# Optimization experiments

Measured on AMD Instinct MI355X. Metric: run time of the kernel, lower is better.

The kernel has to match this reference:

```python
import jax, jax.numpy as jnp
import numpy as np
from jax import lax

N_SAMPLES = 2 ** 15      # 32768
D_SIZE = 256             # number of dictionary atoms
KERNEL = 256             # atom length
N_STEPS = 16             # sparse_coding_iterations
CHANNELS = 128


def setup_inputs() -> dict:
    key = jax.random.key(0)
    ks = jax.random.split(key, 9)
    B = 8
    x = jax.random.normal(ks[0], (B, N_SAMPLES), dtype=jnp.float32)
    # dictionary, initialized uniform(-1, 1) as in nn.Parameter(...).uniform_(-1, 1)
    d = jax.random.uniform(ks[1], (D_SIZE, KERNEL), dtype=jnp.float32, minval=-1.0, maxval=1.0)
    # 1x1 Conv1d weights stored as (out, in); biases (out,)
    w_pos_amp = jax.random.normal(ks[2], (CHANNELS, 2), dtype=jnp.float32) * 0.1
    b_pos_amp = jnp.zeros((CHANNELS,), dtype=jnp.float32)
    w_atoms = jax.random.normal(ks[3], (CHANNELS, D_SIZE), dtype=jnp.float32) * 0.05
    b_atoms = jnp.zeros((CHANNELS,), dtype=jnp.float32)
    w_reduce = jax.random.normal(ks[4], (CHANNELS, 2 * CHANNELS), dtype=jnp.float32) * 0.05
    b_reduce = jnp.zeros((CHANNELS,), dtype=jnp.float32)
    return {
        'x': x, 'd': d,
        'w_pos_amp': w_pos_amp, 'b_pos_amp': b_pos_amp,
        'w_atoms': w_atoms, 'b_atoms': b_atoms,
        'w_reduce': w_reduce, 'b_reduce': b_reduce,
    }


def _correlate(residual, d):
    # residual: (B, 1, N), d: (D, K) -> feature map (B, D, N-K+1) (valid cross-correlation,
    # identical to torch F.conv1d with no padding)
    return lax.conv_general_dilated(
        residual, d[:, None, :], window_strides=(1,), padding='VALID',
        dimension_numbers=('NCH', 'OIH', 'NCH'))


def _matching_pursuit(x3, d):
    """16-step greedy matching pursuit. Returns key points (B, 2+D, N_STEPS) and residual."""
    B = x3.shape[0]
    T = N_SAMPLES - KERNEL + 1  # valid correlation length

    def step(residual, _):
        fm = _correlate(residual, d)                       # (B, D, T)
        flat = fm.reshape(B, -1)
        idx = jnp.argmax(jnp.abs(flat), axis=1)            # best (atom, pos) per example
        amp = jnp.take_along_axis(flat, idx[:, None], axis=1)[:, 0]
        atom_idx = idx // T
        pos = idx % T

        def subtract(r, p, ai, a):
            seg = lax.dynamic_slice(r, (p,), (KERNEL,))
            return lax.dynamic_update_slice(r, seg - a * d[ai], (p,))

        new_res = jax.vmap(subtract)(residual[:, 0, :], pos, atom_idx, amp)[:, None, :]
        enc = jnp.concatenate([
            (pos.astype(jnp.float32) / T)[:, None],        # normalized position
            amp[:, None],                                  # amplitude
            jax.nn.one_hot(atom_idx, D_SIZE, dtype=jnp.float32),  # atom one-hot
        ], axis=1)                                         # (B, 2+D)
        return new_res, enc

    residual, encs = lax.scan(step, x3, None, length=N_STEPS)  # encs: (S, B, 2+D)
    kp = jnp.transpose(encs, (1, 2, 0))                        # (B, 2+D, S)
    return kp, residual


def _conv1x1(w, b, x):
    # w: (O, C), x: (B, C, T) -> (B, O, T)
    return jnp.einsum('oc,bct->bot', w, x) + b[None, :, None]


def reference(x, d, w_pos_amp, b_pos_amp, w_atoms, b_atoms, w_reduce, b_reduce):
    B = x.shape[0]
    x3 = x.reshape(B, 1, N_SAMPLES)
    kp, _ = _matching_pursuit(x3, d)          # (B, 258, 16)
    pos_amp = kp[:, :2, :]
    atoms = kp[:, 2:, :]
    pa = _conv1x1(w_pos_amp, b_pos_amp, pos_amp)
    at = _conv1x1(w_atoms, b_atoms, atoms)
    h = jnp.concatenate([pa, at], axis=1)     # (B, 2*channels, 16)
    return _conv1x1(w_reduce, b_reduce, h)    # (B, channels, 16)
```

## Files before the change

kernel.cpp:

```cpp
#include <hip/hip_runtime.h>
#include <hip/hip_bf16.h>
#include <float.h>

#define NS 32768
#define KER 256
#define TOUT 32513
#define NATOM 256
#define NSTEP 16
#define BATCH 8
#define NBLK 255
#define XSTR 33024
#define SW4(i) ((i) + (((i) >> 5) << 2))

typedef __attribute__((ext_vector_type(8))) _Float16 half8;
typedef __attribute__((ext_vector_type(16))) float f32x16;
typedef __attribute__((ext_vector_type(4))) unsigned int uint4v;
typedef unsigned long long u64;

__device__ __forceinline__ void cmax(float& ba, float& bs, float& bi,
                                     float oa, float os, float oi) {
    if (oa > ba || (oa == ba && oi < bi)) { ba = oa; bs = os; bi = oi; }
}

__device__ __forceinline__ u64 packkey(float sig, int idx) {
    return ((u64)__float_as_uint(fabsf(sig)) << 32)
         | ((u64)((0x7FFFFFu - (unsigned int)idx) << 1))
         | (u64)(__float_as_uint(sig) >> 31);
}
__device__ __forceinline__ void unpackkey(u64 k, float& sig, int& idx) {
    const float av = __uint_as_float((unsigned int)(k >> 32));
    const unsigned int lo = (unsigned int)k;
    idx = 0x7FFFFF - (int)((lo >> 1) & 0x7FFFFFu);
    sig = (lo & 1u) ? -av : av;
}

__device__ __forceinline__ void fma8(float acc[8], float4 dA, float4 dB,
                                     float4 w0, float4 w1, float4 w2, float4 w3) {
    float w[16] = {w0.x,w0.y,w0.z,w0.w, w1.x,w1.y,w1.z,w1.w,
                   w2.x,w2.y,w2.z,w2.w, w3.x,w3.y,w3.z,w3.w};
    float dv[8] = {dA.x,dA.y,dA.z,dA.w, dB.x,dB.y,dB.z,dB.w};
#pragma unroll
    for (int i = 0; i < 8; ++i)
#pragma unroll
        for (int j = 0; j < 8; ++j)
            acc[j] = fmaf(dv[i], w[i + j], acc[j]);
}

__device__ __forceinline__ unsigned short f16hi(float v) {
    return __builtin_bit_cast(unsigned short, (_Float16)v);
}
__device__ __forceinline__ unsigned short f16lo(float v) {
    const _Float16 h = (_Float16)v;
    return __builtin_bit_cast(unsigned short, (_Float16)(v - (float)h));
}

__global__ __launch_bounds__(256) void k_prep(const float* __restrict__ x,
                                              const float* __restrict__ d,
                                              uint4* __restrict__ xhl4,
                                              uint4* __restrict__ dhF,
                                              uint4* __restrict__ dlF) {
    const int gid = blockIdx.x * 256 + threadIdx.x;
    const int NXE = BATCH * XSTR;
    if (gid < NXE) {
        const int b = gid / XSTR, i = gid - b * XSTR;
        float v[4];
#pragma unroll
        for (int u = 0; u < 4; ++u)
            v[u] = (i + u < NS) ? x[b * NS + i + u] : 0.f;
        uint4 q;
        q.x = (unsigned int)f16hi(v[0]) | ((unsigned int)f16hi(v[1]) << 16);
        q.y = (unsigned int)f16hi(v[2]) | ((unsigned int)f16hi(v[3]) << 16);
        q.z = (unsigned int)f16lo(v[0]) | ((unsigned int)f16lo(v[1]) << 16);
        q.w = (unsigned int)f16lo(v[2]) | ((unsigned int)f16lo(v[3]) << 16);
        xhl4[gid] = q;
    } else {
        const int j = gid - NXE;
        if (j < NATOM * 32) {
            const int kg = j >> 8, atom = j & 255;
            const float* dp = d + atom * 256 + (kg << 3);
            uint4 hw, lw;
            hw.x = (unsigned int)f16hi(dp[0]) | ((unsigned int)f16hi(dp[1]) << 16);
            hw.y = (unsigned int)f16hi(dp[2]) | ((unsigned int)f16hi(dp[3]) << 16);
            hw.z = (unsigned int)f16hi(dp[4]) | ((unsigned int)f16hi(dp[5]) << 16);
            hw.w = (unsigned int)f16hi(dp[6]) | ((unsigned int)f16hi(dp[7]) << 16);
            lw.x = (unsigned int)f16lo(dp[0]) | ((unsigned int)f16lo(dp[1]) << 16);
            lw.y = (unsigned int)f16lo(dp[2]) | ((unsigned int)f16lo(dp[3]) << 16);
            lw.z = (unsigned int)f16lo(dp[4]) | ((unsigned int)f16lo(dp[5]) << 16);
            lw.w = (unsigned int)f16lo(dp[6]) | ((unsigned int)f16lo(dp[7]) << 16);
            dhF[(kg << 8) + atom] = hw;
            dlF[(kg << 8) + atom] = lw;
        }
    }
}

__global__ __launch_bounds__(256) void k_init(const uint4* __restrict__ xhl4,
                                              const uint4* __restrict__ dhF,
                                              const uint4* __restrict__ dlF,
                                              float2* __restrict__ bm,
                                              u64* __restrict__ l2k) {
    const int c = blockIdx.x, mg = blockIdx.y, b = blockIdx.z;
    const int tid = threadIdx.x;
    const int w = tid >> 6, l = tid & 63;
    const int n = l & 31, h = l >> 5;
    __shared__ uint4 xw[512];
    __shared__ u64 wmax[4][32];
    const int t0 = c << 8;
    xw[tid] = xhl4[b * XSTR + t0 + tid];
    xw[tid + 256] = xhl4[b * XSTR + t0 + 256 + tid];
    __syncthreads();

    f32x16 acc00, acc01;
#pragma unroll
    for (int j = 0; j < 16; ++j) { acc00[j] = 0.f; acc01[j] = 0.f; }

    const int abase = (mg << 5) + n;
    const int sbb = (w << 6) + n + (h << 3);

    half8 fbh[4], fbl[4];
    {
        const uint4 q0 = xw[sbb], q1 = xw[sbb + 4];
        const uint4v hv = {q0.x, q0.y, q1.x, q1.y};
        const uint4v lv = {q0.z, q0.w, q1.z, q1.w};
        fbh[0] = __builtin_bit_cast(half8, hv);
        fbl[0] = __builtin_bit_cast(half8, lv);
    }
    {
        const uint4 q0 = xw[sbb + 16], q1 = xw[sbb + 20];
        const uint4v hv = {q0.x, q0.y, q1.x, q1.y};
        const uint4v lv = {q0.z, q0.w, q1.z, q1.w};
        fbh[1] = __builtin_bit_cast(half8, hv);
        fbl[1] = __builtin_bit_cast(half8, lv);
    }

#pragma unroll 4
    for (int kk = 0; kk < 16; ++kk) {
        const int kg = (kk << 1) + h;
        const half8 ah0 = __builtin_bit_cast(half8, dhF[(kg << 8) + abase]);
        const half8 al0 = __builtin_bit_cast(half8, dlF[(kg << 8) + abase]);
        {
            const int sN = sbb + ((kk + 2) << 4);
            const uint4 q0 = xw[sN], q1 = xw[sN + 4];
            const uint4v hv = {q0.x, q0.y, q1.x, q1.y};
            const uint4v lv = {q0.z, q0.w, q1.z, q1.w};
            fbh[(kk + 2) & 3] = __builtin_bit_cast(half8, hv);
            fbl[(kk + 2) & 3] = __builtin_bit_cast(half8, lv);
        }
        const half8 b0h = fbh[kk & 3],       b0l = fbl[kk & 3];
        const half8 b1h = fbh[(kk + 2) & 3], b1l = fbl[(kk + 2) & 3];
        acc00 = __builtin_amdgcn_mfma_f32_32x32x16_f16(ah0, b0l, acc00, 0, 0, 0);
        acc00 = __builtin_amdgcn_mfma_f32_32x32x16_f16(al0, b0h, acc00, 0, 0, 0);
        acc00 = __builtin_amdgcn_mfma_f32_32x32x16_f16(ah0, b0h, acc00, 0, 0, 0);
        acc01 = __builtin_amdgcn_mfma_f32_32x32x16_f16(ah0, b1l, acc01, 0, 0, 0);
        acc01 = __builtin_amdgcn_mfma_f32_32x32x16_f16(al0, b1h, acc01, 0, 0, 0);
        acc01 = __builtin_amdgcn_mfma_f32_32x32x16_f16(ah0, b1h, acc01, 0, 0, 0);
    }

    const int tb = t0 + (w << 6) + n;
#pragma unroll
    for (int r = 0; r < 16; ++r) {
        const int amt = (r & 3) + ((r >> 2) << 3) + (h << 2);
        const int idx0 = ((mg << 5) + amt) * TOUT + tb;
        const float v0 = acc00[r], v1 = acc01[r];
        const unsigned int c0 = (0x7FFFFFu - (unsigned int)idx0);
        u64 k0 = 0ull, k1 = 0ull;
        if (tb < TOUT)
            k0 = ((u64)__float_as_uint(fabsf(v0)) << 32)
               | ((u64)(c0 << 1))
               | (u64)(__float_as_uint(v0) >> 31);
        if (tb + 32 < TOUT)
            k1 = ((u64)__float_as_uint(fabsf(v1)) << 32)
               | ((u64)((c0 - 32u) << 1))
               | (u64)(__float_as_uint(v1) >> 31);
        u64 k = (k1 > k0) ? k1 : k0;
#pragma unroll
        for (int m = 1; m <= 16; m <<= 1) {
            const u64 ok = __shfl_xor(k, m, 32);
            if (ok > k) k = ok;
        }
        if (n == 0) wmax[w][amt] = k;
    }
    __syncthreads();
    if (tid < 64) {
        const int a = tid & 31, p = tid >> 5;
        u64 k = wmax[(p << 1)][a];
        const u64 k2 = wmax[(p << 1) + 1][a];
        if (k2 > k) k = k2;
        const int blk = (c << 1) + p;
        const int atom = (mg << 5) + a;
        if (blk < NBLK) {
            float bsg; int idx;
            unpackkey(k, bsg, idx);
            bm[(size_t)((b << 8) + atom) * NBLK + blk] =
                make_float2(bsg, (float)idx);
            atomicMax(&l2k[(b << 8) + atom], k);
        }
    }
}

__global__ __launch_bounds__(512) void k_step(const float* __restrict__ d,
                                              const float* __restrict__ resid_src,
                                              float* __restrict__ resid_dst,
                                              float2* __restrict__ bm,
                                              u64* __restrict__ l2,
                                              int* __restrict__ pos_a,
                                              int* __restrict__ atom_a,
                                              float* __restrict__ amp_a,
                                              int step) {
    const int og = blockIdx.x, b = blockIdx.y;
    const int tid = threadIdx.x;
    const int wave = tid >> 6, lane = tid & 63;
    __shared__ float dt[2048];
    __shared__ float rsu[1024];
    __shared__ u64 sred[8];
    __shared__ float4 upd[8][5];
    __shared__ int sh_pos, sh_atom, sh_prev;
    __shared__ float sh_amp;

    ((float4*)dt)[tid] = ((const float4*)(d + og * 2048))[tid];
    if (tid == 0 && step >= 2) sh_prev = pos_a[(step - 1) * BATCH + b];
    u64* l2r = l2 + (step & 1) * (BATCH * NATOM);
    u64* l2w = l2 + ((step + 1) & 1) * (BATCH * NATOM);

    {
        u64 k = 0ull;
        if (tid < 256) k = l2r[(b << 8) + tid];
#pragma unroll
        for (int m = 1; m <= 32; m <<= 1) {
            const u64 ok = __shfl_xor(k, m);
            if (ok > k) k = ok;
        }
        if (lane == 0) sred[wave] = k;
    }
    __syncthreads();
    if (tid == 0) {
        u64 k = sred[0];
#pragma unroll
        for (int i = 1; i < 8; ++i) if (sred[i] > k) k = sred[i];
        float sig; int idx;
        unpackkey(k, sig, idx);
        const int atom = idx / TOUT;
        const int pos = idx - atom * TOUT;
        sh_pos = pos; sh_atom = atom; sh_amp = sig;
        if (og == 0) {
            pos_a[step * BATCH + b] = pos;
            atom_a[step * BATCH + b] = atom;
            amp_a[step * BATCH + b] = sig;
        }
    }
    __syncthreads();
    const int p = sh_pos, atom_s = sh_atom;
    const float amp = sh_amp;

    if (step < 2) {
        for (int i = tid; i < 1024; i += 512) {
            const int g = (og << 10) + i;
            float v = resid_src[(size_t)b * NS + g];
            const int off = g - p;
            if (off >= 0 && off < KER)
                v = __fsub_rn(v, __fmul_rn(amp, d[atom_s * KER + off]));
            resid_dst[(size_t)b * NS + g] = v;
        }
    } else if (og == 0) {
        if (tid < 256) {
            const int g = p + tid;
            resid_dst[(size_t)b * NS + g] =
                __fsub_rn(resid_src[(size_t)b * NS + g],
                          __fmul_rn(amp, d[atom_s * KER + tid]));
        } else {
            const int g = sh_prev + (tid - 256);
            if (g < p || g > p + 255)
                resid_dst[(size_t)b * NS + g] = resid_src[(size_t)b * NS + g];
        }
    }

    int tlo = p - 255; if (tlo < 0) tlo = 0;
    int thi = p + 255; if (thi > TOUT - 1) thi = TOUT - 1;
    const int bs0 = tlo >> 7, be0 = thi >> 7;
    const int rbase = bs0 << 7;
    const int nblks = be0 - bs0 + 1;
    const int rlen = (nblks << 7) + 255;
    for (int i = tid; i < rlen; i += 512) {
        const int g = rbase + i;
        float v = (g < NS) ? resid_src[(size_t)b * NS + g] : 0.f;
        const int off = g - p;
        if (g < NS && off >= 0 && off < KER)
            v = __fsub_rn(v, __fmul_rn(amp, d[atom_s * KER + off]));
        rsu[SW4(i)] = v;
    }
    __syncthreads();

    const int lg = lane >> 4, l16 = lane & 15;
    const float* dp = dt + (wave << 8) + (lg << 6);
    const int atomg = (og << 3) + wave;
    for (int bb = 0; bb < nblks; ++bb) {
        const int blk = bs0 + bb;
        const int t0r = (bb << 7) + (l16 << 3) + (lg << 6);
        float acc[8];
#pragma unroll
        for (int j = 0; j < 8; ++j) acc[j] = 0.f;
        float4 A0 = *(const float4*)(rsu + SW4(t0r));
        float4 A1 = *(const float4*)(rsu + SW4(t0r + 4));
        float4 B0 = *(const float4*)(rsu + SW4(t0r + 8));
        float4 B1 = *(const float4*)(rsu + SW4(t0r + 12));
#pragma unroll
        for (int kk = 0; kk < 64; kk += 16) {
            const float4 d0 = *(const float4*)(dp + kk);
            const float4 d1 = *(const float4*)(dp + kk + 4);
            const float4 N0 = *(const float4*)(rsu + SW4(t0r + kk + 16));
            const float4 N1 = *(const float4*)(rsu + SW4(t0r + kk + 20));
            fma8(acc, d0, d1, A0, A1, B0, B1);
            const float4 d2 = *(const float4*)(dp + kk + 8);
            const float4 d3 = *(const float4*)(dp + kk + 12);
            const float4 M0 = *(const float4*)(rsu + SW4(t0r + kk + 24));
            const float4 M1 = *(const float4*)(rsu + SW4(t0r + kk + 28));
            fma8(acc, d2, d3, B0, B1, N0, N1);
            A0 = N0; A1 = N1; B0 = M0; B1 = M1;
        }
#pragma unroll
        for (int j = 0; j < 8; ++j) {
            acc[j] += __shfl_xor(acc[j], 16);
            acc[j] += __shfl_xor(acc[j], 32);
        }
        float ba = -1.f, bsg = 0.f, bi = 3.0e7f;
        const int tbp = rbase + (bb << 7) + (l16 << 3);
#pragma unroll
        for (int j = 0; j < 8; ++j) {
            const int t = tbp + j;
            const float av = fabsf(acc[j]);
            if (t < TOUT && av > ba) { ba = av; bsg = acc[j]; bi = (float)(atomg * TOUT + t); }
        }
#pragma unroll
        for (int m = 32; m >= 1; m >>= 1) {
            const float oa = __shfl_xor(ba, m);
            const float os = __shfl_xor(bsg, m);
            const float oi = __shfl_xor(bi, m);
            cmax(ba, bsg, bi, oa, os, oi);
        }
        if (lane == 0) {
            bm[(size_t)(b * NATOM + atomg) * NBLK + blk] = make_float2(bsg, bi);
            upd[wave][bb] = make_float4(ba, bsg, bi, 0.f);
        }
    }
    __syncthreads();

    {
        const u64 ko = l2r[(b << 8) + atomg];
        float eox; int eidx;
        unpackkey(ko, eox, eidx);
        const int oblk = (eidx - atomg * TOUT) >> 7;
        if (oblk >= bs0 && oblk <= be0) {
            float ba = -1.f, bsg = 0.f, bi = 3.0e7f;
            const float2* row = bm + (size_t)(b * NATOM + atomg) * NBLK;
            for (int i = lane; i < NBLK; i += 64) {
                if (i >= bs0 && i <= be0) {
                    const float4 e2 = upd[wave][i - bs0];
                    cmax(ba, bsg, bi, e2.x, e2.y, e2.z);
                } else {
                    const float2 e2 = row[i];
                    cmax(ba, bsg, bi, fabsf(e2.x), e2.x, e2.y);
                }
            }
#pragma unroll
            for (int m = 32; m >= 1; m >>= 1) {
                const float oa = __shfl_xor(ba, m);
                const float os = __shfl_xor(bsg, m);
                const float oi = __shfl_xor(bi, m);
                cmax(ba, bsg, bi, oa, os, oi);
            }
            if (lane == 0) l2w[(b << 8) + atomg] = packkey(bsg, (int)bi);
        } else if (lane == 0) {
            u64 k = ko;
            for (int bb = 0; bb < nblks; ++bb) {
                const float4 e2 = upd[wave][bb];
                const u64 ku = packkey(e2.y, (int)e2.z);
                if (ku > k) k = ku;
            }
            l2w[(b << 8) + atomg] = k;
        }
    }
}

__global__ __launch_bounds__(128) void k_head(const int* __restrict__ pos_a,
                                              const int* __restrict__ atom_a,
                                              const float* __restrict__ amp_a,
                                              const u64* __restrict__ l2,
                                              const float* __restrict__ wpa,
                                              const float* __restrict__ bpa,
                                              const float* __restrict__ wat,
                                              const float* __restrict__ bat,
                                              const float* __restrict__ wr,
                                              const float* __restrict__ br,
                                              float* __restrict__ out) {
    const int s = blockIdx.x, b = blockIdx.y;
    const int o = threadIdx.x;
    __shared__ u64 hred[2];
    __shared__ int sh_pos, sh_atom;
    __shared__ float sh_amp;
    int pos, atom; float amp;
    if (s == NSTEP - 1) {
        const u64* l2r = l2 + ((NSTEP - 1) & 1) * (BATCH * NATOM);
        u64 k = l2r[(b << 8) + o];
        const u64 k2 = l2r[(b << 8) + 128 + o];
        if (k2 > k) k = k2;
#pragma unroll
        for (int m = 1; m <= 32; m <<= 1) {
            const u64 ok = __shfl_xor(k, m);
            if (ok > k) k = ok;
        }
        if ((o & 63) == 0) hred[o >> 6] = k;
        __syncthreads();
        if (o == 0) {
            u64 r = hred[0];
            if (hred[1] > r) r = hred[1];
            float sig; int idx;
            unpackkey(r, sig, idx);
            sh_atom = idx / TOUT;
            sh_pos = idx - sh_atom * TOUT;
            sh_amp = sig;
        }
        __syncthreads();
        pos = sh_pos; atom = sh_atom; amp = sh_amp;
    } else {
        pos  = pos_a[s * BATCH + b];
        atom = atom_a[s * BATCH + b];
        amp  = amp_a[s * BATCH + b];
    }
    const float posn = (float)pos / 32513.0f;
    float sum = br[o];
    for (int c = 0; c < 128; ++c) {
        const float pa = wpa[c * 2] * posn + wpa[c * 2 + 1] * amp + bpa[c];
        const float at = wat[c * 256 + atom] + bat[c];
        sum += wr[o * 256 + c] * pa + wr[o * 256 + 128 + c] * at;
    }
    out[(b * 128 + o) * NSTEP + s] = sum;
}

extern "C" void kernel_launch(void* const* d_in, const int* in_sizes, int n_in,
                              void* d_out, int out_size, void* d_ws, size_t ws_size,
                              hipStream_t stream) {
    const float* x   = (const float*)d_in[0];
    const float* d   = (const float*)d_in[1];
    const float* wpa = (const float*)d_in[2];
    const float* bpa = (const float*)d_in[3];
    const float* wat = (const float*)d_in[4];
    const float* bat = (const float*)d_in[5];
    const float* wr  = (const float*)d_in[6];
    const float* br  = (const float*)d_in[7];
    float* out = (float*)d_out;

    char* ws = (char*)d_ws;
    float2* bm    = (float2*)ws;
    u64*    l2k   = (u64*)(ws + 4177920);
    int*    pos_a  = (int*)(ws + 4210688);
    int*    atom_a = (int*)(ws + 4211200);
    float*  amp_a  = (float*)(ws + 4211712);
    uint4*  dhF    = (uint4*)(ws + 4212224);
    uint4*  dlF    = (uint4*)(ws + 4343296);
    uint4*  xhl4   = (uint4*)(ws + 4474368);
    float*  resid0 = (float*)(ws + 4474368);
    float*  resid1 = (float*)(ws + 5522944);

    hipMemsetAsync(l2k, 0, 32768, stream);
    const int prep_n = BATCH * XSTR + NATOM * 32;
    k_prep<<<(prep_n + 255) / 256, 256, 0, stream>>>(x, d, xhl4, dhF, dlF);
    k_init<<<dim3(128, 8, 8), 256, 0, stream>>>(xhl4, dhF, dlF, bm, l2k);
    for (int st = 0; st < NSTEP - 1; ++st) {
        const float* rs = (st == 0) ? x : ((st & 1) ? resid1 : resid0);
        float* rd = (st & 1) ? resid0 : resid1;
        k_step<<<dim3(32, 8), 512, 0, stream>>>(d, rs, rd, bm, l2k,
                                                pos_a, atom_a, amp_a, st);
    }
    k_head<<<dim3(16, 8), 128, 0, stream>>>(pos_a, atom_a, amp_a, l2k,
                                            wpa, bpa, wat, bat, wr, br, out);
}
```

Measured before the change: 407.5 us.

## Fuse x split into init kernel and double atoms per block

The fp16 hi/lo split of the input signal moves out of the prep kernel and into the init correlation kernel, which now reads raw fp32 x into shared memory and converts it there. This removes the global xhl4 intermediate buffer and its write/read traffic. Each init block now computes 64 atoms instead of 32, reusing the signal tile across twice the MFMAs and halving the grid. The per-block max reduction now goes through a padded shared-memory key table instead of warp shuffles, and atomics are issued only for nonzero keys. The cost is more accumulator registers and a larger shared-memory footprint per block.

```diff
diff --git a/kernel.cpp b/kernel.cpp
--- a/kernel.cpp
+++ b/kernel.cpp
@@ -9,8 +9,8 @@
 #define NSTEP 16
 #define BATCH 8
 #define NBLK 255
-#define XSTR 33024
 #define SW4(i) ((i) + (((i) >> 5) << 2))
+#define KW 1060
 
 typedef __attribute__((ext_vector_type(8))) _Float16 half8;
 typedef __attribute__((ext_vector_type(16))) float f32x16;
@@ -46,54 +46,36 @@
             acc[j] = fmaf(dv[i], w[i + j], acc[j]);
 }
 
-__device__ __forceinline__ unsigned short f16hi(float v) {
-    return __builtin_bit_cast(unsigned short, (_Float16)v);
-}
-__device__ __forceinline__ unsigned short f16lo(float v) {
+__device__ __forceinline__ unsigned int f16hi(float v) {
+    return (unsigned int)__builtin_bit_cast(unsigned short, (_Float16)v);
+}
+__device__ __forceinline__ unsigned int f16lo(float v) {
     const _Float16 h = (_Float16)v;
-    return __builtin_bit_cast(unsigned short, (_Float16)(v - (float)h));
-}
-
-__global__ __launch_bounds__(256) void k_prep(const float* __restrict__ x,
-                                              const float* __restrict__ d,
-                                              uint4* __restrict__ xhl4,
+    return (unsigned int)__builtin_bit_cast(unsigned short, (_Float16)(v - (float)h));
+}
+
+__global__ __launch_bounds__(256) void k_prep(const float* __restrict__ d,
                                               uint4* __restrict__ dhF,
                                               uint4* __restrict__ dlF) {
-    const int gid = blockIdx.x * 256 + threadIdx.x;
-    const int NXE = BATCH * XSTR;
-    if (gid < NXE) {
-        const int b = gid / XSTR, i = gid - b * XSTR;
-        float v[4];
-#pragma unroll
-        for (int u = 0; u < 4; ++u)
-            v[u] = (i + u < NS) ? x[b * NS + i + u] : 0.f;
-        uint4 q;
-        q.x = (unsigned int)f16hi(v[0]) | ((unsigned int)f16hi(v[1]) << 16);
-        q.y = (unsigned int)f16hi(v[2]) | ((unsigned int)f16hi(v[3]) << 16);
-        q.z = (unsigned int)f16lo(v[0]) | ((unsigned int)f16lo(v[1]) << 16);
-        q.w = (unsigned int)f16lo(v[2]) | ((unsigned int)f16lo(v[3]) << 16);
-        xhl4[gid] = q;
-    } else {
-        const int j = gid - NXE;
-        if (j < NATOM * 32) {
-            const int kg = j >> 8, atom = j & 255;
-            const float* dp = d + atom * 256 + (kg << 3);
-            uint4 hw, lw;
-            hw.x = (unsigned int)f16hi(dp[0]) | ((unsigned int)f16hi(dp[1]) << 16);
-            hw.y = (unsigned int)f16hi(dp[2]) | ((unsigned int)f16hi(dp[3]) << 16);
-            hw.z = (unsigned int)f16hi(dp[4]) | ((unsigned int)f16hi(dp[5]) << 16);
-            hw.w = (unsigned int)f16hi(dp[6]) | ((unsigned int)f16hi(dp[7]) << 16);
-            lw.x = (unsigned int)f16lo(dp[0]) | ((unsigned int)f16lo(dp[1]) << 16);
-            lw.y = (unsigned int)f16lo(dp[2]) | ((unsigned int)f16lo(dp[3]) << 16);
-            lw.z = (unsigned int)f16lo(dp[4]) | ((unsigned int)f16lo(dp[5]) << 16);
-            lw.w = (unsigned int)f16lo(dp[6]) | ((unsigned int)f16lo(dp[7]) << 16);
-            dhF[(kg << 8) + atom] = hw;
-            dlF[(kg << 8) + atom] = lw;
-        }
-    }
-}
-
-__global__ __launch_bounds__(256) void k_init(const uint4* __restrict__ xhl4,
+    const int j = blockIdx.x * 256 + threadIdx.x;
+    if (j < NATOM * 32) {
+        const int kg = j >> 8, atom = j & 255;
+        const float* dp = d + atom * 256 + (kg << 3);
+        uint4 hw, lw;
+        hw.x = f16hi(dp[0]) | (f16hi(dp[1]) << 16);
+        hw.y = f16hi(dp[2]) | (f16hi(dp[3]) << 16);
+        hw.z = f16hi(dp[4]) | (f16hi(dp[5]) << 16);
+        hw.w = f16hi(dp[6]) | (f16hi(dp[7]) << 16);
+        lw.x = f16lo(dp[0]) | (f16lo(dp[1]) << 16);
+        lw.y = f16lo(dp[2]) | (f16lo(dp[3]) << 16);
+        lw.z = f16lo(dp[4]) | (f16lo(dp[5]) << 16);
+        lw.w = f16lo(dp[6]) | (f16lo(dp[7]) << 16);
+        dhF[(kg << 8) + atom] = hw;
+        dlF[(kg << 8) + atom] = lw;
+    }
+}
+
+__global__ __launch_bounds__(256) void k_init(const float* __restrict__ x,
                                               const uint4* __restrict__ dhF,
                                               const uint4* __restrict__ dlF,
                                               float2* __restrict__ bm,
@@ -102,18 +84,41 @@
     const int tid = threadIdx.x;
     const int w = tid >> 6, l = tid & 63;
     const int n = l & 31, h = l >> 5;
+    __shared__ float xs[520];
     __shared__ uint4 xw[512];
-    __shared__ u64 wmax[4][32];
+    __shared__ u64 keyL[4 * KW];
     const int t0 = c << 8;
-    xw[tid] = xhl4[b * XSTR + t0 + tid];
-    xw[tid + 256] = xhl4[b * XSTR + t0 + 256 + tid];
-    __syncthreads();
-
-    f32x16 acc00, acc01;
-#pragma unroll
-    for (int j = 0; j < 16; ++j) { acc00[j] = 0.f; acc01[j] = 0.f; }
-
-    const int abase = (mg << 5) + n;
+    const float* xp = x + (size_t)b * NS;
+    for (int i4 = tid; i4 < 130; i4 += 256) {
+        const int i = i4 << 2, g = t0 + i;
+        float4 v;
+        if (g + 3 < NS) v = *(const float4*)(xp + g);
+        else {
+            v.x = (g     < NS) ? xp[g]     : 0.f;
+            v.y = (g + 1 < NS) ? xp[g + 1] : 0.f;
+            v.z = (g + 2 < NS) ? xp[g + 2] : 0.f;
+            v.w = (g + 3 < NS) ? xp[g + 3] : 0.f;
+        }
+        *(float4*)(xs + i) = v;
+    }
+    __syncthreads();
+    for (int i = tid; i < 512; i += 256) {
+        const float v0 = xs[i], v1 = xs[i + 1], v2 = xs[i + 2], v3 = xs[i + 3];
+        uint4 q;
+        q.x = f16hi(v0) | (f16hi(v1) << 16);
+        q.y = f16hi(v2) | (f16hi(v3) << 16);
+        q.z = f16lo(v0) | (f16lo(v1) << 16);
+        q.w = f16lo(v2) | (f16lo(v3) << 16);
+        xw[i] = q;
+    }
+    __syncthreads();
+
+    f32x16 acc00, acc01, acc10, acc11;
+#pragma unroll
+    for (int j = 0; j < 16; ++j) { acc00[j] = 0.f; acc01[j] = 0.f;
+                                   acc10[j] = 0.f; acc11[j] = 0.f; }
+
+    const int abase = (mg << 6) + n;
     const int sbb = (w << 6) + n + (h << 3);
 
     half8 fbh[4], fbl[4];
@@ -137,6 +142,8 @@
         const int kg = (kk << 1) + h;
         const half8 ah0 = __builtin_bit_cast(half8, dhF[(kg << 8) + abase]);
         const half8 al0 = __builtin_bit_cast(half8, dlF[(kg << 8) + abase]);
+        const half8 ah1 = __builtin_bit_cast(half8, dhF[(kg << 8) + abase + 32]);
+        const half8 al1 = __builtin_bit_cast(half8, dlF[(kg << 8) + abase + 32]);
         {
             const int sN = sbb + ((kk + 2) << 4);
             const uint4 q0 = xw[sN], q1 = xw[sN + 4];
@@ -150,50 +157,69 @@
         acc00 = __builtin_amdgcn_mfma_f32_32x32x16_f16(ah0, b0l, acc00, 0, 0, 0);
         acc00 = __builtin_amdgcn_mfma_f32_32x32x16_f16(al0, b0h, acc00, 0, 0, 0);
         acc00 = __builtin_amdgcn_mfma_f32_32x32x16_f16(ah0, b0h, acc00, 0, 0, 0);
+        acc10 = __builtin_amdgcn_mfma_f32_32x32x16_f16(ah1, b0l, acc10, 0, 0, 0);
+        acc10 = __builtin_amdgcn_mfma_f32_32x32x16_f16(al1, b0h, acc10, 0, 0, 0);
+        acc10 = __builtin_amdgcn_mfma_f32_32x32x16_f16(ah1, b0h, acc10, 0, 0, 0);
         acc01 = __builtin_amdgcn_mfma_f32_32x32x16_f16(ah0, b1l, acc01, 0, 0, 0);
         acc01 = __builtin_amdgcn_mfma_f32_32x32x16_f16(al0, b1h, acc01, 0, 0, 0);
         acc01 = __builtin_amdgcn_mfma_f32_32x32x16_f16(ah0, b1h, acc01, 0, 0, 0);
+        acc11 = __builtin_amdgcn_mfma_f32_32x32x16_f16(ah1, b1l, acc11, 0, 0, 0);
+        acc11 = __builtin_amdgcn_mfma_f32_32x32x16_f16(al1, b1h, acc11, 0, 0, 0);
+        acc11 = __builtin_amdgcn_mfma_f32_32x32x16_f16(ah1, b1h, acc11, 0, 0, 0);
     }
 
     const int tb = t0 + (w << 6) + n;
 #pragma unroll
-    for (int r = 0; r < 16; ++r) {
-        const int amt = (r & 3) + ((r >> 2) << 3) + (h << 2);
-        const int idx0 = ((mg << 5) + amt) * TOUT + tb;
-        const float v0 = acc00[r], v1 = acc01[r];
-        const unsigned int c0 = (0x7FFFFFu - (unsigned int)idx0);
-        u64 k0 = 0ull, k1 = 0ull;
-        if (tb < TOUT)
-            k0 = ((u64)__float_as_uint(fabsf(v0)) << 32)
-               | ((u64)(c0 << 1))
-               | (u64)(__float_as_uint(v0) >> 31);
-        if (tb + 32 < TOUT)
-            k1 = ((u64)__float_as_uint(fabsf(v1)) << 32)
-               | ((u64)((c0 - 32u) << 1))
-               | (u64)(__float_as_uint(v1) >> 31);
-        u64 k = (k1 > k0) ? k1 : k0;
-#pragma unroll
-        for (int m = 1; m <= 16; m <<= 1) {
-            const u64 ok = __shfl_xor(k, m, 32);
-            if (ok > k) k = ok;
-        }
-        if (n == 0) wmax[w][amt] = k;
-    }
-    __syncthreads();
-    if (tid < 64) {
-        const int a = tid & 31, p = tid >> 5;
-        u64 k = wmax[(p << 1)][a];
-        const u64 k2 = wmax[(p << 1) + 1][a];
-        if (k2 > k) k = k2;
-        const int blk = (c << 1) + p;
-        const int atom = (mg << 5) + a;
-        if (blk < NBLK) {
-            float bsg; int idx;
-            unpackkey(k, bsg, idx);
-            bm[(size_t)((b << 8) + atom) * NBLK + blk] =
-                make_float2(bsg, (float)idx);
-            atomicMax(&l2k[(b << 8) + atom], k);
-        }
+    for (int mt = 0; mt < 2; ++mt) {
+#pragma unroll
+        for (int r = 0; r < 16; ++r) {
+            const int amt = (r & 3) + ((r >> 2) << 3) + (h << 2);
+            const int idx0 = ((mg << 6) + (mt << 5) + amt) * TOUT + tb;
+            const float v0 = (mt == 0) ? acc00[r] : acc10[r];
+            const float v1 = (mt == 0) ? acc01[r] : acc11[r];
+            const unsigned int c0 = (0x7FFFFFu - (unsigned int)idx0);
+            u64 k0 = 0ull, k1 = 0ull;
+            if (tb < TOUT)
+                k0 = ((u64)__float_as_uint(fabsf(v0)) << 32)
+                   | ((u64)(c0 << 1))
+                   | (u64)(__float_as_uint(v0) >> 31);
+            if (tb + 32 < TOUT)
+                k1 = ((u64)__float_as_uint(fabsf(v1)) << 32)
+                   | ((u64)((c0 - 32u) << 1))
+                   | (u64)(__float_as_uint(v1) >> 31);
+            keyL[w * KW + amt * 33 + n] = (k1 > k0) ? k1 : k0;
+        }
+        __syncthreads();
+        {
+            const int inst = tid >> 2, sub = tid & 3;
+            const int p2 = inst & 1, amt = inst >> 1;
+            u64 k = 0ull;
+#pragma unroll
+            for (int j = 0; j < 16; ++j) {
+                const int e = sub * 16 + j;
+                const u64 ke = keyL[((p2 << 1) + (e >> 5)) * KW + amt * 33 + (e & 31)];
+                if (ke > k) k = ke;
+            }
+#pragma unroll
+            for (int m = 1; m <= 2; m <<= 1) {
+                const u64 ok = __shfl_xor(k, m, 4);
+                if (ok > k) k = ok;
+            }
+            const int blk = (c << 1) + p2;
+            const int atom = (mg << 6) + (mt << 5) + amt;
+            if (sub == 0 && blk < NBLK) {
+                float bsg; int idx;
+                unpackkey(k, bsg, idx);
+                bm[(size_t)((b << 8) + atom) * NBLK + blk] =
+                    make_float2(bsg, (float)idx);
+            }
+            const u64 op = __shfl_xor(k, 4, 8);
+            if ((tid & 7) == 0) {
+                const u64 km = (op > k) ? op : k;
+                if (km) atomicMax(&l2k[(b << 8) + atom], km);
+            }
+        }
+        __syncthreads();
     }
 }
 
@@ -456,14 +482,12 @@
     float*  amp_a  = (float*)(ws + 4211712);
     uint4*  dhF    = (uint4*)(ws + 4212224);
     uint4*  dlF    = (uint4*)(ws + 4343296);
-    uint4*  xhl4   = (uint4*)(ws + 4474368);
     float*  resid0 = (float*)(ws + 4474368);
     float*  resid1 = (float*)(ws + 5522944);
 
     hipMemsetAsync(l2k, 0, 32768, stream);
-    const int prep_n = BATCH * XSTR + NATOM * 32;
-    k_prep<<<(prep_n + 255) / 256, 256, 0, stream>>>(x, d, xhl4, dhF, dlF);
-    k_init<<<dim3(128, 8, 8), 256, 0, stream>>>(xhl4, dhF, dlF, bm, l2k);
+    k_prep<<<32, 256, 0, stream>>>(d, dhF, dlF);
+    k_init<<<dim3(128, 4, 8), 256, 0, stream>>>(x, dhF, dlF, bm, l2k);
     for (int st = 0; st < NSTEP - 1; ++st) {
         const float* rs = (st == 0) ? x : ((st & 1) ? resid1 : resid0);
         float* rd = (st & 1) ? resid0 : resid1;
```

Result: faster. 373.7 us (-8.3%).
